# Performance work log

Measured on AMD Instinct MI355X. Metric: run time of the kernel, lower is better.

The kernel has to match this reference:

```python
import jax, jax.numpy as jnp
import numpy as np

BN_EPS = 1e-5
K = 9  # 3x3 kernel positions


def conv2d(x, w, b, pad, dil=1):
    out = jax.lax.conv_general_dilated(
        x, w, window_strides=(1, 1), padding=((pad, pad), (pad, pad)),
        rhs_dilation=(dil, dil), dimension_numbers=('NCHW', 'OIHW', 'NCHW'))
    return out + b[None, :, None, None]


def bn_relu(x, g, be, mu, var):
    inv = jax.lax.rsqrt(var + BN_EPS)
    return jax.nn.relu((x - mu[None, :, None, None]) * (g * inv)[None, :, None, None] + be[None, :, None, None])


def deform_conv(x, w_om, b_om, w, b):
    # DCNv2-style modulated deformable 3x3 conv, stride 1, pad 1, dg=1.
    B, C, H, W = x.shape
    om = conv2d(x, w_om, b_om, pad=1)               # [B, 27, H, W]
    o1, o2, m = jnp.split(om, 3, axis=1)            # dy, dx, mask logits: [B,9,H,W]
    mask = jax.nn.sigmoid(m)
    ky, kx = jnp.meshgrid(jnp.arange(3), jnp.arange(3), indexing='ij')
    ky = (ky.reshape(-1) - 1).astype(x.dtype)       # kernel offsets in {-1,0,1}
    kx = (kx.reshape(-1) - 1).astype(x.dtype)
    py = jnp.arange(H, dtype=x.dtype)[None, None, :, None] + ky[None, :, None, None] + o1  # [B,9,H,W]
    px = jnp.arange(W, dtype=x.dtype)[None, None, None, :] + kx[None, :, None, None] + o2

    y0 = jnp.floor(py); x0 = jnp.floor(px)
    wy1 = py - y0; wx1 = px - x0
    y0i = y0.astype(jnp.int32); x0i = x0.astype(jnp.int32)
    x_flat = x.reshape(B, C, H * W)

    def corner(yi, xi, wgt):
        valid = ((yi >= 0) & (yi < H) & (xi >= 0) & (xi < W)).astype(x.dtype)
        idx = jnp.clip(yi, 0, H - 1) * W + jnp.clip(xi, 0, W - 1)      # [B,9,H,W]
        g = jax.vmap(lambda xf, i: xf[:, i])(x_flat, idx.reshape(B, -1))
        g = g.reshape(B, C, K, H, W)
        return g * (wgt * valid)[:, None]

    cols = (corner(y0i,     x0i,     (1 - wy1) * (1 - wx1))
            + corner(y0i,     x0i + 1, (1 - wy1) * wx1)
            + corner(y0i + 1, x0i,     wy1 * (1 - wx1))
            + corner(y0i + 1, x0i + 1, wy1 * wx1))                       # [B,C,9,H,W]
    cols = cols * mask[:, None]
    out = jnp.einsum('bckhw,ock->bohw', cols, w.reshape(w.shape[0], C, K))
    return out + b[None, :, None, None]


def setup_inputs() -> dict:
    key = jax.random.key(0)
    ks = jax.random.split(key, 24)
    B, C, H, W = 2, 64, 256, 256
    d = {}
    d['x'] = jax.random.normal(ks[0], (B, C, H, W), jnp.float32)
    d['w_om'] = jax.random.normal(ks[1], (27, C, 3, 3), jnp.float32) * 0.01
    d['b_om'] = jax.random.normal(ks[2], (27,), jnp.float32) * 0.01
    d['w_dcn'] = jax.random.normal(ks[3], (C, C, 3, 3), jnp.float32) * 0.05
    d['b_dcn'] = jax.random.normal(ks[4], (C,), jnp.float32) * 0.05
    for i, pfx in enumerate(['bn1', 'bn2', 'bn3']):
        d[pfx + '_g'] = jax.random.uniform(ks[5 + 4 * i], (C,), jnp.float32, 0.5, 1.5)
        d[pfx + '_b'] = jax.random.normal(ks[6 + 4 * i], (C,), jnp.float32) * 0.05
        d[pfx + '_m'] = jax.random.normal(ks[7 + 4 * i], (C,), jnp.float32) * 0.05
        d[pfx + '_v'] = jax.random.uniform(ks[8 + 4 * i], (C,), jnp.float32, 0.5, 1.5)
    d['w_h'] = jax.random.normal(ks[17], (C, C, 3, 3), jnp.float32) * 0.05
    d['b_h'] = jax.random.normal(ks[18], (C,), jnp.float32) * 0.05
    d['w_w'] = jax.random.normal(ks[19], (C, C, 3, 3), jnp.float32) * 0.05
    d['b_w'] = jax.random.normal(ks[20], (C,), jnp.float32) * 0.05
    d['w3'] = jax.random.normal(ks[21], (1, C, 3, 3), jnp.float32) * 0.05
    d['b3'] = jax.random.normal(ks[22], (1,), jnp.float32) * 0.05
    return d


def reference(x, w_om, b_om, w_dcn, b_dcn,
              bn1_g, bn1_b, bn1_m, bn1_v,
              w_h, b_h, bn2_g, bn2_b, bn2_m, bn2_v,
              w_w, b_w, bn3_g, bn3_b, bn3_m, bn3_v,
              w3, b3):
    h = deform_conv(x, w_om, b_om, w_dcn, b_dcn)
    h = bn_relu(h, bn1_g, bn1_b, bn1_m, bn1_v)
    h = conv2d(h, w_h, b_h, pad=2, dil=2)
    h = bn_relu(h, bn2_g, bn2_b, bn2_m, bn2_v)
    h = conv2d(h, w_w, b_w, pad=2, dil=2)
    h = bn_relu(h, bn3_g, bn3_b, bn3_m, bn3_v)
    h = conv2d(h, w3, b3, pad=1)
    return jnp.clip(jax.nn.sigmoid(h), 1e-4, 1.0 - 1e-4)
```

## Files before the change

kernel.cpp:

```cpp
#include <hip/hip_runtime.h>
#include <math.h>

#define HH 256
#define WW 256
#define HW (HH*WW)
#define NPX (2*HW)

typedef __attribute__((ext_vector_type(8))) short bf16x8;
typedef __attribute__((ext_vector_type(4))) float f32x4;

__device__ __forceinline__ float bf2f(short h) {
    union { unsigned u; float f; } v; v.u = ((unsigned)(unsigned short)h) << 16; return v.f;
}
__device__ __forceinline__ short f2bf(float f) {
    union { float f; unsigned u; } v; v.f = f;
    unsigned r = v.u + 0x7fffu + ((v.u >> 16) & 1u);
    return (short)(r >> 16);
}
__device__ __forceinline__ short f2bf_fast(float f) {
    union { float f; unsigned u; } v; v.f = f;
    return (short)((v.u + 0x8000u) >> 16);
}

__global__ __launch_bounds__(256) void k_prep_w(
        const float* __restrict__ w_om, const float* __restrict__ w_dcn,
        const float* __restrict__ w_h,  const float* __restrict__ w_w,
        const float* __restrict__ w3,
        short* __restrict__ wt_om, short* __restrict__ wt_dcn,
        short* __restrict__ wt_h,  short* __restrict__ wt_w,
        float* __restrict__ w3t) {
    int i = blockIdx.x * 256 + threadIdx.x;
    if (i >= 64 * 576) return;
    int o = i / 576, k = i - o * 576, t = k >> 6, c = k & 63;
    int kb = k >> 3, j = k & 7;
    int src = (o * 64 + c) * 9 + t;
    int dst = (kb * 64 + o) * 8 + j;
    wt_dcn[dst] = f2bf(w_dcn[src]);
    wt_h[dst]   = f2bf(w_h[src]);
    wt_w[dst]   = f2bf(w_w[src]);
    if (o < 32) wt_om[(kb * 32 + o) * 8 + j] = (o < 27) ? f2bf(w_om[src]) : (short)0;
    if (o == 0) w3t[k] = w3[c * 9 + t];
}

__global__ __launch_bounds__(256) void k_x2cl(const float* __restrict__ x,
        short* __restrict__ xcl) {
    __shared__ short tile[256 * 66];
    const int xx = threadIdx.x;
    const int row = blockIdx.x;
    const int b = row >> 8, y = row & 255;
    for (int c = 0; c < 64; ++c)
        tile[xx * 66 + c] = f2bf(x[((b * 64 + c) << 16) + (y << 8) + xx]);
    __syncthreads();
    short* op = xcl + ((row << 8) + xx) * 64;
#pragma unroll
    for (int j = 0; j < 8; ++j) {
        bf16x8 v;
#pragma unroll
        for (int e = 0; e < 8; ++e) v[e] = tile[xx * 66 + j * 8 + e];
        *(bf16x8*)(op + j * 8) = v;
    }
}

#define XPS 72

__global__ __launch_bounds__(256) __attribute__((amdgpu_waves_per_eu(2, 4)))
void k_om_mfma(const short* __restrict__ xcl,
        const short* __restrict__ wt, const float* __restrict__ b_om,
        float* __restrict__ om_px) {
    __shared__ short xt[180 * XPS];
    const int lane = threadIdx.x & 63, wave = threadIdx.x >> 6;
    const int quad = lane >> 4, l16 = lane & 15;
    const int tIdx = (blockIdx.x & 7) * 128 + (blockIdx.x >> 3);
    const int tr = tIdx >> 4, tc = tIdx & 15;
    const int b = tr >> 5;
    const int ty0 = (tr & 31) * 8, tx0 = tc * 16;
    const int base = b << 16;
    if (threadIdx.x < 180) {
        const int p = threadIdx.x;
        const int sy = ty0 - 1 + p / 18, sx = tx0 - 1 + p % 18;
        short* dst = &xt[p * XPS];
        if (((unsigned)sy < 256u) && ((unsigned)sx < 256u)) {
            const short* src = xcl + (size_t)((base + sy * 256 + sx) * 64);
#pragma unroll
            for (int j = 0; j < 8; ++j)
                *(bf16x8*)(dst + j * 8) = *(const bf16x8*)(src + j * 8);
        } else {
            bf16x8 z = {0,0,0,0,0,0,0,0};
#pragma unroll
            for (int j = 0; j < 8; ++j) *(bf16x8*)(dst + j * 8) = z;
        }
    }
    __syncthreads();
    const int ly = wave * 2;
    f32x4 acc[2][2];
#pragma unroll
    for (int h = 0; h < 2; ++h)
#pragma unroll
        for (int g = 0; g < 2; ++g) acc[h][g] = (f32x4){0,0,0,0};

    auto loadB = [&](int s, bf16x8* Bv) {
        const int kb = s * 4 + quad;
#pragma unroll
        for (int g = 0; g < 2; ++g)
            Bv[g] = *(const bf16x8*)(wt + (kb * 32 + g * 16 + l16) * 8);
    };
    bf16x8 B[2][2];
    loadB(0, B[0]);
#pragma unroll
    for (int s = 0; s < 18; ++s) {
        if (s < 17) loadB(s + 1, B[(s + 1) & 1]);
        const int t = s >> 1, c0 = (s & 1) * 32;
        const int dy = t / 3 - 1, dx = t % 3 - 1;
        const int cidx = c0 + quad * 8;
        bf16x8 a0 = *(const bf16x8*)&xt[((ly + 1 + dy) * 18 + (l16 + 1 + dx)) * XPS + cidx];
        bf16x8 a1 = *(const bf16x8*)&xt[((ly + 2 + dy) * 18 + (l16 + 1 + dx)) * XPS + cidx];
#pragma unroll
        for (int g = 0; g < 2; ++g) {
            acc[0][g] = __builtin_amdgcn_mfma_f32_16x16x32_bf16(a0, B[s & 1][g], acc[0][g], 0, 0, 0);
            acc[1][g] = __builtin_amdgcn_mfma_f32_16x16x32_bf16(a1, B[s & 1][g], acc[1][g], 0, 0, 0);
        }
    }
#pragma unroll
    for (int h = 0; h < 2; ++h)
#pragma unroll
    for (int g = 0; g < 2; ++g) {
        int o = g * 16 + l16;
        float bo = (o < 27) ? b_om[o] : 0.f;
#pragma unroll
        for (int r = 0; r < 4; ++r) {
            int pix = base + ((ty0 + ly + h) << 8) + tx0 + quad * 4 + r;
            float v = acc[h][g][r] + bo;
            if (o >= 18 && o < 27) v = 1.f / (1.f + expf(-v));
            om_px[(size_t)pix * 32 + o] = v;
        }
    }
}

__global__ __launch_bounds__(256) __attribute__((amdgpu_waves_per_eu(2, 4)))
void k_dcn_mfma(const short* __restrict__ xcl,
        const float* __restrict__ om_px, const short* __restrict__ wt,
        const float* __restrict__ bias,
        const float* __restrict__ gg, const float* __restrict__ be,
        const float* __restrict__ mu, const float* __restrict__ var,
        short* __restrict__ out_cl) {
    __shared__ short xt[256 * XPS];
    const int lane = threadIdx.x & 63, wave = threadIdx.x >> 6;
    const int quad = lane >> 4, l16 = lane & 15;
    const int band = blockIdx.x & 7, idx = blockIdx.x >> 3;
    const int tr = band * 8 + (idx >> 5), tc = idx & 31;
    const int b = tr >> 5;
    const int ty0 = (tr & 31) * 8, tx0 = tc * 8;
    const int base = b << 16;
    const int hy0 = ty0 - 4, hx0 = tx0 - 4;
    {
        const int p = threadIdx.x;
        const int sy = min(max(hy0 + (p >> 4), 0), 255);
        const int sx = min(max(hx0 + (p & 15), 0), 255);
        const short* src = xcl + (size_t)((base + sy * 256 + sx) * 64);
        short* dst = &xt[p * XPS];
#pragma unroll
        for (int j = 0; j < 8; ++j)
            *(bf16x8*)(dst + j * 8) = *(const bf16x8*)(src + j * 8);
    }
    __syncthreads();

    const int y = ty0 + wave * 2 + (l16 >> 3);
    const int x = tx0 + (l16 & 7);
    const int gpx = base + (y << 8) + x;
    f32x4 acc[4];
#pragma unroll
    for (int i = 0; i < 4; ++i) acc[i] = (f32x4){0,0,0,0};

    const f32x4* omv4 = (const f32x4*)(om_px + (size_t)gpx * 32);
    float omr[27];
#pragma unroll
    for (int i = 0; i < 7; ++i) {
        f32x4 v = omv4[i];
#pragma unroll
        for (int e = 0; e < 4; ++e) { int j = i * 4 + e; if (j < 27) omr[j] = v[e]; }
    }

#pragma unroll
    for (int t = 0; t < 9; ++t) {
        const int ky = t / 3 - 1, kx = t % 3 - 1;
        float o1 = omr[t], o2 = omr[9 + t], m = omr[18 + t];
        float py = (float)(y + ky) + o1;
        float px = (float)(x + kx) + o2;
        float y0f = floorf(py), x0f = floorf(px);
        float wy1 = py - y0f, wx1 = px - x0f;
        int y0 = (int)y0f, xi0 = (int)x0f, y1 = y0 + 1, xi1 = xi0 + 1;
        float w00 = (1.f - wy1) * (1.f - wx1) * m;
        float w01 = (1.f - wy1) * wx1 * m;
        float w10 = wy1 * (1.f - wx1) * m;
        float w11 = wy1 * wx1 * m;
        if (!((unsigned)y0  < 256u)) { w00 = 0.f; w01 = 0.f; }
        if (!((unsigned)y1  < 256u)) { w10 = 0.f; w11 = 0.f; }
        if (!((unsigned)xi0 < 256u)) { w00 = 0.f; w10 = 0.f; }
        if (!((unsigned)xi1 < 256u)) { w01 = 0.f; w11 = 0.f; }
        int cy0 = min(max(y0, 0), 255), cy1 = min(max(y1, 0), 255);
        int cx0 = min(max(xi0, 0), 255), cx1 = min(max(xi1, 0), 255);
        int iy0 = cy0 - hy0, iy1 = cy1 - hy0;
        int ix0 = cx0 - hx0, ix1 = cx1 - hx0;
        bool inh = ((unsigned)iy0 < 16u) && ((unsigned)iy1 < 16u)
                && ((unsigned)ix0 < 16u) && ((unsigned)ix1 < 16u);

        bf16x8 C[2][4];
        if (__all(inh)) {
            const int p00 = (iy0 * 16 + ix0) * XPS, p01 = (iy0 * 16 + ix1) * XPS;
            const int p10 = (iy1 * 16 + ix0) * XPS, p11 = (iy1 * 16 + ix1) * XPS;
#pragma unroll
            for (int h = 0; h < 2; ++h) {
                const int cb = h * 32 + quad * 8;
                C[h][0] = *(const bf16x8*)&xt[p00 + cb];
                C[h][1] = *(const bf16x8*)&xt[p01 + cb];
                C[h][2] = *(const bf16x8*)&xt[p10 + cb];
                C[h][3] = *(const bf16x8*)&xt[p11 + cb];
            }
        } else {
            const int i00 = (base + cy0 * 256 + cx0) * 64;
            const int i01 = (base + cy0 * 256 + cx1) * 64;
            const int i10 = (base + cy1 * 256 + cx0) * 64;
            const int i11 = (base + cy1 * 256 + cx1) * 64;
#pragma unroll
            for (int h = 0; h < 2; ++h) {
                const int cb = h * 32 + quad * 8;
                C[h][0] = *(const bf16x8*)(xcl + i00 + cb);
                C[h][1] = *(const bf16x8*)(xcl + i01 + cb);
                C[h][2] = *(const bf16x8*)(xcl + i10 + cb);
                C[h][3] = *(const bf16x8*)(xcl + i11 + cb);
            }
        }
#pragma unroll
        for (int h = 0; h < 2; ++h) {
            bf16x8 av;
#pragma unroll
            for (int e = 0; e < 8; ++e) {
                float s = w00 * bf2f(C[h][0][e]) + w01 * bf2f(C[h][1][e])
                        + w10 * bf2f(C[h][2][e]) + w11 * bf2f(C[h][3][e]);
                av[e] = f2bf_fast(s);
            }
            const int kb = t * 8 + h * 4 + quad;
#pragma unroll
            for (int g = 0; g < 4; ++g) {
                bf16x8 bv = *(const bf16x8*)(wt + (kb * 64 + g * 16 + l16) * 8);
                acc[g] = __builtin_amdgcn_mfma_f32_16x16x32_bf16(av, bv, acc[g], 0, 0, 0);
            }
        }
    }
#pragma unroll
    for (int g = 0; g < 4; ++g) {
        int o = g * 16 + l16;
        float sc = gg[o] * rsqrtf(var[o] + 1e-5f);
        float off = (bias[o] - mu[o]) * sc + be[o];
#pragma unroll
        for (int r = 0; r < 4; ++r) {
            int mm = quad * 4 + r;
            int pix = base + ((ty0 + wave * 2 + (mm >> 3)) << 8) + tx0 + (mm & 7);
            float v = acc[g][r] * sc + off;
            out_cl[(size_t)pix * 64 + o] = f2bf(fmaxf(v, 0.f));
        }
    }
}

__global__ __launch_bounds__(256) __attribute__((amdgpu_waves_per_eu(2, 4)))
void k_conv_mfma(const short* __restrict__ in_cl,
        const short* __restrict__ wt, const float* __restrict__ bias,
        const float* __restrict__ gg, const float* __restrict__ be,
        const float* __restrict__ mu, const float* __restrict__ var,
        short* __restrict__ out_cl) {
    __shared__ short xt[240 * XPS];
    const int lane = threadIdx.x & 63, wave = threadIdx.x >> 6;
    const int quad = lane >> 4, l16 = lane & 15;
    const int tIdx = (blockIdx.x & 7) * 128 + (blockIdx.x >> 3);
    const int tr = tIdx >> 4, tc = tIdx & 15;
    const int b = tr >> 5;
    const int ty0 = (tr & 31) * 8, tx0 = tc * 16;
    const int base = b << 16;
    if (threadIdx.x < 240) {
        const int p = threadIdx.x;
        const int sy = ty0 - 2 + p / 20, sx = tx0 - 2 + p % 20;
        short* dst = &xt[p * XPS];
        if (((unsigned)sy < 256u) && ((unsigned)sx < 256u)) {
            const short* src = in_cl + (size_t)((base + sy * 256 + sx) * 64);
#pragma unroll
            for (int j = 0; j < 8; ++j)
                *(bf16x8*)(dst + j * 8) = *(const bf16x8*)(src + j * 8);
        } else {
            bf16x8 z = {0,0,0,0,0,0,0,0};
#pragma unroll
            for (int j = 0; j < 8; ++j) *(bf16x8*)(dst + j * 8) = z;
        }
    }
    __syncthreads();
    const int ly = wave * 2;
    f32x4 acc[2][4];
#pragma unroll
    for (int h = 0; h < 2; ++h)
#pragma unroll
        for (int g = 0; g < 4; ++g) acc[h][g] = (f32x4){0,0,0,0};

    auto loadB = [&](int s, bf16x8* Bv) {
        const int kb = s * 4 + quad;
#pragma unroll
        for (int g = 0; g < 4; ++g)
            Bv[g] = *(const bf16x8*)(wt + (kb * 64 + g * 16 + l16) * 8);
    };
    bf16x8 B[2][4];
    loadB(0, B[0]);
#pragma unroll
    for (int s = 0; s < 18; ++s) {
        if (s < 17) loadB(s + 1, B[(s + 1) & 1]);
        const int t = s >> 1, c0 = (s & 1) * 32;
        const int dy = (t / 3 - 1) * 2, dx = (t % 3 - 1) * 2;
        const int cidx = c0 + quad * 8;
        bf16x8 a0 = *(const bf16x8*)&xt[((ly + 2 + dy) * 20 + (l16 + 2 + dx)) * XPS + cidx];
        bf16x8 a1 = *(const bf16x8*)&xt[((ly + 3 + dy) * 20 + (l16 + 2 + dx)) * XPS + cidx];
#pragma unroll
        for (int g = 0; g < 4; ++g) {
            acc[0][g] = __builtin_amdgcn_mfma_f32_16x16x32_bf16(a0, B[s & 1][g], acc[0][g], 0, 0, 0);
            acc[1][g] = __builtin_amdgcn_mfma_f32_16x16x32_bf16(a1, B[s & 1][g], acc[1][g], 0, 0, 0);
        }
    }
#pragma unroll
    for (int h = 0; h < 2; ++h)
#pragma unroll
    for (int g = 0; g < 4; ++g) {
        int o = g * 16 + l16;
        float sc = gg[o] * rsqrtf(var[o] + 1e-5f);
        float off = (bias[o] - mu[o]) * sc + be[o];
#pragma unroll
        for (int r = 0; r < 4; ++r) {
            int pix = base + ((ty0 + ly + h) << 8) + tx0 + quad * 4 + r;
            float v = acc[h][g][r] * sc + off;
            out_cl[(size_t)pix * 64 + o] = f2bf(fmaxf(v, 0.f));
        }
    }
}

__global__ __launch_bounds__(256) void k_final(const short* __restrict__ h_cl,
        const float* __restrict__ w3t, const float* __restrict__ b3,
        float* __restrict__ out) {
    __shared__ short xt[324 * XPS];
    const int tIdx = (blockIdx.x & 7) * 64 + (blockIdx.x >> 3);
    const int tr = tIdx >> 4, tc = tIdx & 15;
    const int b = tr >> 4;
    const int ty0 = (tr & 15) * 16, tx0 = tc * 16;
    const int base = b << 16;
    for (int p = threadIdx.x; p < 324; p += 256) {
        const int sy = ty0 - 1 + p / 18, sx = tx0 - 1 + p % 18;
        short* dst = &xt[p * XPS];
        if (((unsigned)sy < 256u) && ((unsigned)sx < 256u)) {
            const short* src = h_cl + (size_t)((base + sy * 256 + sx) * 64);
#pragma unroll
            for (int j = 0; j < 8; ++j)
                *(bf16x8*)(dst + j * 8) = *(const bf16x8*)(src + j * 8);
        } else {
            bf16x8 z = {0,0,0,0,0,0,0,0};
#pragma unroll
            for (int j = 0; j < 8; ++j) *(bf16x8*)(dst + j * 8) = z;
        }
    }
    __syncthreads();
    const int ly = threadIdx.x >> 4, lx = threadIdx.x & 15;
    float acc = 0.f;
#pragma unroll
    for (int t = 0; t < 9; ++t) {
        const int hidx = (ly + 1 + t / 3 - 1) * 18 + (lx + 1 + t % 3 - 1);
        const short* hp = &xt[hidx * XPS];
        const float* wp = w3t + t * 64;
#pragma unroll
        for (int j = 0; j < 64; j += 8) {
            bf16x8 v = *(const bf16x8*)(hp + j);
#pragma unroll
            for (int e = 0; e < 8; ++e)
                acc = fmaf(bf2f(v[e]), wp[j + e], acc);
        }
    }
    float s = 1.f / (1.f + expf(-(acc + b3[0])));
    out[base + ((ty0 + ly) << 8) + tx0 + lx] = fminf(fmaxf(s, 1e-4f), 1.f - 1e-4f);
}

extern "C" void kernel_launch(void* const* d_in, const int* in_sizes, int n_in,
                              void* d_out, int out_size, void* d_ws, size_t ws_size,
                              hipStream_t stream) {
    const float* x     = (const float*)d_in[0];
    const float* w_om  = (const float*)d_in[1];
    const float* b_om  = (const float*)d_in[2];
    const float* w_dcn = (const float*)d_in[3];
    const float* b_dcn = (const float*)d_in[4];
    const float* bn1g = (const float*)d_in[5],  *bn1b = (const float*)d_in[6];
    const float* bn1m = (const float*)d_in[7],  *bn1v = (const float*)d_in[8];
    const float* bn2g = (const float*)d_in[9],  *bn2b = (const float*)d_in[10];
    const float* bn2m = (const float*)d_in[11], *bn2v = (const float*)d_in[12];
    const float* bn3g = (const float*)d_in[13], *bn3b = (const float*)d_in[14];
    const float* bn3m = (const float*)d_in[15], *bn3v = (const float*)d_in[16];
    const float* w_h = (const float*)d_in[17], *b_h = (const float*)d_in[18];
    const float* w_w = (const float*)d_in[19], *b_w = (const float*)d_in[20];
    const float* w3  = (const float*)d_in[21], *b3  = (const float*)d_in[22];
    float* outp = (float*)d_out;

    char* ws = (char*)d_ws;
    float* om_px = (float*)ws;
    short* xcl   = (short*)(ws + (size_t)NPX * 32 * 4);
    short* h1    = xcl + (size_t)NPX * 64;
    short* h2    = h1 + (size_t)NPX * 64;
    short* wt_om  = h2 + (size_t)NPX * 64;
    short* wt_dcn = wt_om  + 32 * 576;
    short* wt_h   = wt_dcn + 64 * 576;
    short* wt_w   = wt_h   + 64 * 576;
    float* w3t    = (float*)(wt_w + 64 * 576);

    dim3 blk(256);
    k_prep_w<<<(64 * 576 + 255) / 256, blk, 0, stream>>>(
        w_om, w_dcn, w_h, w_w, w3, wt_om, wt_dcn, wt_h, wt_w, w3t);
    k_x2cl<<<512, blk, 0, stream>>>(x, xcl);
    k_om_mfma<<<NPX / 128, blk, 0, stream>>>(xcl, wt_om, b_om, om_px);
    k_dcn_mfma<<<NPX / 64, blk, 0, stream>>>(xcl, om_px, wt_dcn, b_dcn,
                                             bn1g, bn1b, bn1m, bn1v, h1);
    k_conv_mfma<<<NPX / 128, blk, 0, stream>>>(h1, wt_h, b_h, bn2g, bn2b, bn2m, bn2v, h2);
    k_conv_mfma<<<NPX / 128, blk, 0, stream>>>(h2, wt_w, b_w, bn3g, bn3b, bn3m, bn3v, h1);
    k_final<<<512, blk, 0, stream>>>(h1, w3t, b3, outp);
}
```

Baseline: 227.3 us.

## Fuse offset/mask conv into deformable conv kernel and triple-buffer conv weights

Removes the separate offset/mask convolution kernel. Each DCN block now computes the 27 offset/mask channels for its 8x8 tile with MFMA from the x halo it already holds in LDS, and stages the results in shared memory instead of a global om_px buffer. This drops one launch and a 32-float-per-pixel global write and read, at the cost of more registers and an extra barrier in the DCN kernel. Separately, the dilated conv kernel prefetches weights two steps ahead with a three-slot buffer rather than two.

Result: faster. 220.1 us (-3.2%).

```diff
diff --git a/kernel.cpp b/kernel.cpp
--- a/kernel.cpp
+++ b/kernel.cpp
@@ -64,86 +64,15 @@
 #define XPS 72
 
 __global__ __launch_bounds__(256) __attribute__((amdgpu_waves_per_eu(2, 4)))
-void k_om_mfma(const short* __restrict__ xcl,
-        const short* __restrict__ wt, const float* __restrict__ b_om,
-        float* __restrict__ om_px) {
-    __shared__ short xt[180 * XPS];
-    const int lane = threadIdx.x & 63, wave = threadIdx.x >> 6;
-    const int quad = lane >> 4, l16 = lane & 15;
-    const int tIdx = (blockIdx.x & 7) * 128 + (blockIdx.x >> 3);
-    const int tr = tIdx >> 4, tc = tIdx & 15;
-    const int b = tr >> 5;
-    const int ty0 = (tr & 31) * 8, tx0 = tc * 16;
-    const int base = b << 16;
-    if (threadIdx.x < 180) {
-        const int p = threadIdx.x;
-        const int sy = ty0 - 1 + p / 18, sx = tx0 - 1 + p % 18;
-        short* dst = &xt[p * XPS];
-        if (((unsigned)sy < 256u) && ((unsigned)sx < 256u)) {
-            const short* src = xcl + (size_t)((base + sy * 256 + sx) * 64);
-#pragma unroll
-            for (int j = 0; j < 8; ++j)
-                *(bf16x8*)(dst + j * 8) = *(const bf16x8*)(src + j * 8);
-        } else {
-            bf16x8 z = {0,0,0,0,0,0,0,0};
-#pragma unroll
-            for (int j = 0; j < 8; ++j) *(bf16x8*)(dst + j * 8) = z;
-        }
-    }
-    __syncthreads();
-    const int ly = wave * 2;
-    f32x4 acc[2][2];
-#pragma unroll
-    for (int h = 0; h < 2; ++h)
-#pragma unroll
-        for (int g = 0; g < 2; ++g) acc[h][g] = (f32x4){0,0,0,0};
-
-    auto loadB = [&](int s, bf16x8* Bv) {
-        const int kb = s * 4 + quad;
-#pragma unroll
-        for (int g = 0; g < 2; ++g)
-            Bv[g] = *(const bf16x8*)(wt + (kb * 32 + g * 16 + l16) * 8);
-    };
-    bf16x8 B[2][2];
-    loadB(0, B[0]);
-#pragma unroll
-    for (int s = 0; s < 18; ++s) {
-        if (s < 17) loadB(s + 1, B[(s + 1) & 1]);
-        const int t = s >> 1, c0 = (s & 1) * 32;
-        const int dy = t / 3 - 1, dx = t % 3 - 1;
-        const int cidx = c0 + quad * 8;
-        bf16x8 a0 = *(const bf16x8*)&xt[((ly + 1 + dy) * 18 + (l16 + 1 + dx)) * XPS + cidx];
-        bf16x8 a1 = *(const bf16x8*)&xt[((ly + 2 + dy) * 18 + (l16 + 1 + dx)) * XPS + cidx];
-#pragma unroll
-        for (int g = 0; g < 2; ++g) {
-            acc[0][g] = __builtin_amdgcn_mfma_f32_16x16x32_bf16(a0, B[s & 1][g], acc[0][g], 0, 0, 0);
-            acc[1][g] = __builtin_amdgcn_mfma_f32_16x16x32_bf16(a1, B[s & 1][g], acc[1][g], 0, 0, 0);
-        }
-    }
-#pragma unroll
-    for (int h = 0; h < 2; ++h)
-#pragma unroll
-    for (int g = 0; g < 2; ++g) {
-        int o = g * 16 + l16;
-        float bo = (o < 27) ? b_om[o] : 0.f;
-#pragma unroll
-        for (int r = 0; r < 4; ++r) {
-            int pix = base + ((ty0 + ly + h) << 8) + tx0 + quad * 4 + r;
-            float v = acc[h][g][r] + bo;
-            if (o >= 18 && o < 27) v = 1.f / (1.f + expf(-v));
-            om_px[(size_t)pix * 32 + o] = v;
-        }
-    }
-}
-
-__global__ __launch_bounds__(256) __attribute__((amdgpu_waves_per_eu(2, 4)))
 void k_dcn_mfma(const short* __restrict__ xcl,
-        const float* __restrict__ om_px, const short* __restrict__ wt,
+        const short* __restrict__ wom, const float* __restrict__ b_om,
+        const short* __restrict__ wt,
         const float* __restrict__ bias,
         const float* __restrict__ gg, const float* __restrict__ be,
         const float* __restrict__ mu, const float* __restrict__ var,
         short* __restrict__ out_cl) {
     __shared__ short xt[256 * XPS];
+    __shared__ float om_lds[64 * 28];
     const int lane = threadIdx.x & 63, wave = threadIdx.x >> 6;
     const int quad = lane >> 4, l16 = lane & 15;
     const int band = blockIdx.x & 7, idx = blockIdx.x >> 3;
@@ -164,14 +93,54 @@
     }
     __syncthreads();
 
-    const int y = ty0 + wave * 2 + (l16 >> 3);
-    const int x = tx0 + (l16 & 7);
-    const int gpx = base + (y << 8) + x;
+    const int lp = wave * 16 + l16;
+    const int pyy = lp >> 3, pxx = lp & 7;
+    const int y = ty0 + pyy, x = tx0 + pxx;
+
+    {
+        f32x4 oacc[2];
+        oacc[0] = (f32x4){0,0,0,0}; oacc[1] = (f32x4){0,0,0,0};
+        auto loadOB = [&](int s, bf16x8* Bv) {
+            const int kb = s * 4 + quad;
+#pragma unroll
+            for (int g = 0; g < 2; ++g)
+                Bv[g] = *(const bf16x8*)(wom + (kb * 32 + g * 16 + l16) * 8);
+        };
+        bf16x8 OB[2][2];
+        loadOB(0, OB[0]);
+#pragma unroll
+        for (int s = 0; s < 18; ++s) {
+            if (s < 17) loadOB(s + 1, OB[(s + 1) & 1]);
+            const int t = s >> 1, c0 = (s & 1) * 32;
+            const int dy = t / 3 - 1, dx = t % 3 - 1;
+            bf16x8 av = *(const bf16x8*)&xt[((pyy + 4 + dy) * 16 + (pxx + 4 + dx)) * XPS + c0 + quad * 8];
+            bool ok = ((unsigned)(y + dy) < 256u) && ((unsigned)(x + dx) < 256u);
+            if (!ok) { bf16x8 z = {0,0,0,0,0,0,0,0}; av = z; }
+#pragma unroll
+            for (int g = 0; g < 2; ++g)
+                oacc[g] = __builtin_amdgcn_mfma_f32_16x16x32_bf16(av, OB[s & 1][g], oacc[g], 0, 0, 0);
+        }
+#pragma unroll
+        for (int g = 0; g < 2; ++g) {
+            int o = g * 16 + l16;
+            if (o < 27) {
+                float bo = b_om[o];
+#pragma unroll
+                for (int r = 0; r < 4; ++r) {
+                    float v = oacc[g][r] + bo;
+                    if (o >= 18) v = 1.f / (1.f + expf(-v));
+                    om_lds[(wave * 16 + quad * 4 + r) * 28 + o] = v;
+                }
+            }
+        }
+    }
+    __syncthreads();
+
     f32x4 acc[4];
 #pragma unroll
     for (int i = 0; i < 4; ++i) acc[i] = (f32x4){0,0,0,0};
 
-    const f32x4* omv4 = (const f32x4*)(om_px + (size_t)gpx * 32);
+    const f32x4* omv4 = (const f32x4*)&om_lds[lp * 28];
     float omr[27];
 #pragma unroll
     for (int i = 0; i < 7; ++i) {
@@ -305,11 +274,12 @@
         for (int g = 0; g < 4; ++g)
             Bv[g] = *(const bf16x8*)(wt + (kb * 64 + g * 16 + l16) * 8);
     };
-    bf16x8 B[2][4];
+    bf16x8 B[3][4];
     loadB(0, B[0]);
+    loadB(1, B[1]);
 #pragma unroll
     for (int s = 0; s < 18; ++s) {
-        if (s < 17) loadB(s + 1, B[(s + 1) & 1]);
+        if (s + 2 < 18) loadB(s + 2, B[(s + 2) % 3]);
         const int t = s >> 1, c0 = (s & 1) * 32;
         const int dy = (t / 3 - 1) * 2, dx = (t % 3 - 1) * 2;
         const int cidx = c0 + quad * 8;
@@ -317,8 +287,8 @@
         bf16x8 a1 = *(const bf16x8*)&xt[((ly + 3 + dy) * 20 + (l16 + 2 + dx)) * XPS + cidx];
 #pragma unroll
         for (int g = 0; g < 4; ++g) {
-            acc[0][g] = __builtin_amdgcn_mfma_f32_16x16x32_bf16(a0, B[s & 1][g], acc[0][g], 0, 0, 0);
-            acc[1][g] = __builtin_amdgcn_mfma_f32_16x16x32_bf16(a1, B[s & 1][g], acc[1][g], 0, 0, 0);
+            acc[0][g] = __builtin_amdgcn_mfma_f32_16x16x32_bf16(a0, B[s % 3][g], acc[0][g], 0, 0, 0);
+            acc[1][g] = __builtin_amdgcn_mfma_f32_16x16x32_bf16(a1, B[s % 3][g], acc[1][g], 0, 0, 0);
         }
     }
 #pragma unroll
@@ -400,8 +370,7 @@
     float* outp = (float*)d_out;
 
     char* ws = (char*)d_ws;
-    float* om_px = (float*)ws;
-    short* xcl   = (short*)(ws + (size_t)NPX * 32 * 4);
+    short* xcl   = (short*)ws;
     short* h1    = xcl + (size_t)NPX * 64;
     short* h2    = h1 + (size_t)NPX * 64;
     short* wt_om  = h2 + (size_t)NPX * 64;
@@ -414,8 +383,7 @@
     k_prep_w<<<(64 * 576 + 255) / 256, blk, 0, stream>>>(
         w_om, w_dcn, w_h, w_w, w3, wt_om, wt_dcn, wt_h, wt_w, w3t);
     k_x2cl<<<512, blk, 0, stream>>>(x, xcl);
-    k_om_mfma<<<NPX / 128, blk, 0, stream>>>(xcl, wt_om, b_om, om_px);
-    k_dcn_mfma<<<NPX / 64, blk, 0, stream>>>(xcl, om_px, wt_dcn, b_dcn,
+    k_dcn_mfma<<<NPX / 64, blk, 0, stream>>>(xcl, wt_om, b_om, wt_dcn, b_dcn,
                                              bn1g, bn1b, bn1m, bn1v, h1);
     k_conv_mfma<<<NPX / 128, blk, 0, stream>>>(h1, wt_h, b_h, bn2g, bn2b, bn2m, bn2v, h2);
     k_conv_mfma<<<NPX / 128, blk, 0, stream>>>(h2, wt_w, b_w, bn3g, bn3b, bn3m, bn3v, h1);
```
